# Performance work log

Hardware: AMD Instinct MI355X
Metric: run time of the kernel (lower is better)

The kernel has to match this reference:

```python
import jax, jax.numpy as jnp
import numpy as np

B, N, D, H = 4, 1024, 512, 8
DH = D // H  # per-head dim for V and for each of the two Q/K halves
LAM = 0.5


def setup_inputs() -> dict:
    key = jax.random.key(0)
    ks = jax.random.split(key, 7)
    s = 0.02
    return {
        "x": jax.random.normal(ks[0], (B, N, D), dtype=jnp.float32),
        "Wq": jax.random.normal(ks[1], (D, 2 * D), dtype=jnp.float32) * s,
        "bq": jax.random.normal(ks[2], (2 * D,), dtype=jnp.float32) * s,
        "Wk": jax.random.normal(ks[3], (D, 2 * D), dtype=jnp.float32) * s,
        "bk": jax.random.normal(ks[4], (2 * D,), dtype=jnp.float32) * s,
        "Wv": jax.random.normal(ks[5], (D, D), dtype=jnp.float32) * s,
        "bv": jax.random.normal(ks[6], (D,), dtype=jnp.float32) * s,
    }


def reference(x, Wq, bq, Wk, bk, Wv, bv):
    b, n, d = x.shape
    q = (x @ Wq + bq).reshape(b, n, H, 2 * DH).transpose(0, 2, 1, 3)  # [B,H,N,2*DH]
    k = (x @ Wk + bk).reshape(b, n, H, 2 * DH).transpose(0, 2, 1, 3)
    v = (x @ Wv + bv).reshape(b, n, H, DH).transpose(0, 2, 1, 3)      # [B,H,N,DH]
    q1, q2 = q[..., :DH], q[..., DH:]
    k1, k2 = k[..., :DH], k[..., DH:]
    scale = 1.0 / jnp.sqrt(jnp.float32(DH))
    a1 = jax.nn.softmax(jnp.einsum("bhqd,bhkd->bhqk", q1, k1) * scale, axis=-1)
    a2 = jax.nn.softmax(jnp.einsum("bhqd,bhkd->bhqk", q2, k2) * scale, axis=-1)
    attn = a1 - LAM * a2                                              # [B,H,N,N]
    out = jnp.einsum("bhqk,bhkd->bhqd", attn, v)                      # [B,H,N,DH]
    return out.transpose(0, 2, 1, 3).reshape(b, n, d)
```

## Files before the change

### kernel.cpp

```cpp
#include <hip/hip_runtime.h>
#include <hip/hip_bf16.h>

typedef unsigned short u16;
typedef short s16x8 __attribute__((ext_vector_type(8)));
typedef float f32x4 __attribute__((ext_vector_type(4)));

__device__ inline u16 f2bf(float f) {
  union { float f; unsigned int u; } v; v.f = f;
  unsigned int r = v.u + 0x7fffu + ((v.u >> 16) & 1u);
  return (u16)(r >> 16);
}

__device__ __forceinline__ void g2lds16(const u16* g, u16* l) {
  __builtin_amdgcn_global_load_lds((const __attribute__((address_space(1))) void*)g,
                                   (__attribute__((address_space(3))) void*)l, 16, 0, 0);
}

__global__ __launch_bounds__(256) void prep_kernel(const float* __restrict__ x,
                                                   const float* __restrict__ Wq,
                                                   const float* __restrict__ Wk,
                                                   const float* __restrict__ Wv,
                                                   u16* __restrict__ xb, u16* __restrict__ wt) {
  __shared__ float tile[64][65];
  int bid = blockIdx.x;
  if (bid < 1024) {
    int i = (bid * 256 + threadIdx.x) * 8;
    float4 a = *(const float4*)(x + i);
    float4 b = *(const float4*)(x + i + 4);
    s16x8 o;
    o[0] = (short)f2bf(a.x); o[1] = (short)f2bf(a.y);
    o[2] = (short)f2bf(a.z); o[3] = (short)f2bf(a.w);
    o[4] = (short)f2bf(b.x); o[5] = (short)f2bf(b.y);
    o[6] = (short)f2bf(b.z); o[7] = (short)f2bf(b.w);
    *(s16x8*)(xb + i) = o;
    return;
  }
  int t = bid - 1024;
  const float* src; int C, rowoff, j0, k0;
  if (t < 256) {
    src = (t < 128) ? Wq : Wk;
    C = 1024; rowoff = (t < 128) ? 0 : 1024;
    int tt = t & 127;
    j0 = (tt & 15) * 64; k0 = (tt >> 4) * 64;
  } else {
    src = Wv; C = 512; rowoff = 2048;
    int tt = t - 256;
    j0 = (tt & 7) * 64; k0 = (tt >> 3) * 64;
  }
  int tx = threadIdx.x % 64, ty4 = threadIdx.x / 64;
#pragma unroll
  for (int p = 0; p < 16; ++p) {
    int r = p * 4 + ty4;
    tile[r][tx] = src[(size_t)(k0 + r) * C + j0 + tx];
  }
  __syncthreads();
#pragma unroll
  for (int p = 0; p < 16; ++p) {
    int r = p * 4 + ty4;
    wt[(size_t)(rowoff + j0 + r) * 512 + k0 + tx] = f2bf(tile[tx][r]);
  }
}

__global__ __launch_bounds__(256, 3) void gemm_qkv(const u16* __restrict__ xb, const u16* __restrict__ wt,
                                                   const float* __restrict__ bq, const float* __restrict__ bk,
                                                   const float* __restrict__ bv,
                                                   u16* __restrict__ qa, u16* __restrict__ ka,
                                                   u16* __restrict__ va) {
  __shared__ __align__(16) u16 As[128 * 64];
  __shared__ __align__(16) u16 Bs[128 * 64];
  int m0 = blockIdx.x * 128, j0 = blockIdx.y * 128;
  int tid = threadIdx.x;
  int w = tid >> 6, lane = tid & 63, quad = lane >> 4, l16 = lane & 15;
  int wr = (w >> 1) * 64, wc = (w & 1) * 64;

  int srow[4], scol[4], sbase[4];
#pragma unroll
  for (int it = 0; it < 4; ++it) {
    int s = it * 256 + tid;
    srow[it] = s >> 3;
    scol[it] = (s & 7) ^ ((s >> 3) & 7);
    sbase[it] = (s & ~63) * 8;
  }

  f32x4 acc[4][4];
#pragma unroll
  for (int i = 0; i < 4; ++i)
#pragma unroll
    for (int j = 0; j < 4; ++j)
#pragma unroll
      for (int r = 0; r < 4; ++r) acc[i][j][r] = 0.f;

  for (int kk = 0; kk < 8; ++kk) {
    int k0 = kk * 64;
    __syncthreads();
#pragma unroll
    for (int it = 0; it < 4; ++it) {
      g2lds16(xb + (size_t)(m0 + srow[it]) * 512 + k0 + scol[it] * 8, &As[sbase[it]]);
      g2lds16(wt + (size_t)(j0 + srow[it]) * 512 + k0 + scol[it] * 8, &Bs[sbase[it]]);
    }
    __syncthreads();
#pragma unroll
    for (int kb = 0; kb < 2; ++kb) {
      s16x8 af[4], bfr[4];
#pragma unroll
      for (int rb = 0; rb < 4; ++rb) {
        int row = wr + rb * 16 + l16;
        af[rb] = *(const s16x8*)(&As[row * 64 + (((kb * 4 + quad) ^ (row & 7)) * 8)]);
      }
#pragma unroll
      for (int cb = 0; cb < 4; ++cb) {
        int row = wc + cb * 16 + l16;
        bfr[cb] = *(const s16x8*)(&Bs[row * 64 + (((kb * 4 + quad) ^ (row & 7)) * 8)]);
      }
#pragma unroll
      for (int rb = 0; rb < 4; ++rb)
#pragma unroll
        for (int cb = 0; cb < 4; ++cb)
          acc[rb][cb] = __builtin_amdgcn_mfma_f32_16x16x32_bf16(af[rb], bfr[cb], acc[rb][cb], 0, 0, 0);
    }
  }

#pragma unroll
  for (int cb = 0; cb < 4; ++cb) {
    int j = j0 + wc + cb * 16 + l16;
    float bias = (j < 1024) ? bq[j] : (j < 2048) ? bk[j - 1024] : bv[j - 2048];
#pragma unroll
    for (int rb = 0; rb < 4; ++rb) {
#pragma unroll
      for (int r = 0; r < 4; ++r) {
        int m = m0 + wr + rb * 16 + quad * 4 + r;
        int bidx = m >> 10, n = m & 1023;
        u16 o = f2bf(acc[rb][cb][r] + bias);
        if (j < 1024) {
          int h = j >> 7, r2 = j & 127;
          qa[((size_t)((bidx * 8 + h) * 1024 + n)) * 128 + r2] = o;
        } else if (j < 2048) {
          int jj = j - 1024, h = jj >> 7, r2 = jj & 127;
          ka[((size_t)((bidx * 8 + h) * 1024 + n)) * 128 + r2] = o;
        } else {
          int jj = j - 2048, h = jj >> 6, d = jj & 63;
          va[((size_t)((bidx * 8 + h) * 64 + d)) * 1024 + n] = o;
        }
      }
    }
  }
}

__global__ __launch_bounds__(256, 2) void attn_kernel(const u16* __restrict__ qa, const u16* __restrict__ ka,
                                                      const u16* __restrict__ va, float* __restrict__ out) {
  __shared__ __align__(16) u16 smem[17408];
  u16* Ks = smem;
  u16* Vs = smem + 8192;
  u16* Ps = smem + 12288;
  float* Ex = (float*)smem;

  int bh = blockIdx.x, b = bh >> 3, h = bh & 7;
  int q0 = blockIdx.y * 32;
  int tid = threadIdx.x, w = tid >> 6, lane = tid & 63, quad = lane >> 4, l16 = lane & 15;
  int kh = w >> 1;
  int qr = q0 + (w & 1) * 16;

  const u16* kgbase = ka + (size_t)bh * 1024 * 128;
  const u16* vgbase = va + (size_t)bh * 64 * 1024;

  const u16* qrow = qa + (size_t)(bh * 1024 + qr + l16) * 128;
  s16x8 qf[2][2];
  qf[0][0] = *(const s16x8*)(qrow + quad * 8);
  qf[0][1] = *(const s16x8*)(qrow + 32 + quad * 8);
  qf[1][0] = *(const s16x8*)(qrow + 64 + quad * 8);
  qf[1][1] = *(const s16x8*)(qrow + 96 + quad * 8);

  f32x4 O1[5], O2[5];
#pragma unroll
  for (int i = 0; i < 5; ++i)
#pragma unroll
    for (int r = 0; r < 4; ++r) { O1[i][r] = 0.f; O2[i][r] = 0.f; }

  s16x8 onesf;
#pragma unroll
  for (int i = 0; i < 8; ++i) onesf[i] = (l16 == 0) ? (short)0x3F80 : (short)0;

  size_t kgo[4]; int kbse[4];
#pragma unroll
  for (int i = 0; i < 4; ++i) {
    int s = i * 256 + tid;
    int skh = s >> 9, row = (s >> 4) & 31, c = s & 15;
    kgo[i] = (size_t)(skh * 512 + row) * 128 + ((c ^ (row & 7)) * 8);
    kbse[i] = (s & ~63) * 8;
  }
  size_t vgo[2]; int vbse[2];
#pragma unroll
  for (int i = 0; i < 2; ++i) {
    int s = i * 256 + tid;
    int skh = s >> 8, row = (s >> 2) & 63, c = s & 3;
    vgo[i] = (size_t)row * 1024 + skh * 512 + ((c ^ (row & 3)) * 8);
    vbse[i] = (s & ~63) * 8;
  }

  for (int kt = 0; kt < 16; ++kt) {
    __syncthreads();
#pragma unroll
    for (int i = 0; i < 4; ++i)
      g2lds16(kgbase + kgo[i] + (size_t)kt * 4096, &Ks[kbse[i]]);
#pragma unroll
    for (int i = 0; i < 2; ++i)
      g2lds16(vgbase + vgo[i] + (size_t)kt * 32, &Vs[vbse[i]]);
    __syncthreads();

    s16x8 vf[4];
#pragma unroll
    for (int ct = 0; ct < 4; ++ct) {
      int row = ct * 16 + l16;
      vf[ct] = *(const s16x8*)(&Vs[kh * 2048 + row * 32 + ((quad ^ (row & 3)) * 8)]);
    }

#pragma unroll
    for (int hh = 0; hh < 2; ++hh) {
#pragma unroll
      for (int nt = 0; nt < 2; ++nt) {
        f32x4 sv; sv[0] = sv[1] = sv[2] = sv[3] = 0.f;
#pragma unroll
        for (int kb = 0; kb < 2; ++kb) {
          int row = nt * 16 + l16;
          s16x8 kf = *(const s16x8*)(&Ks[kh * 4096 + row * 128 +
                                         (((hh * 8 + kb * 4 + quad) ^ (row & 7)) * 8)]);
          sv = __builtin_amdgcn_mfma_f32_16x16x32_bf16(qf[hh][kb], kf, sv, 0, 0, 0);
        }
#pragma unroll
        for (int r = 0; r < 4; ++r)
          Ps[((w * 2 + hh) * 16 + quad * 4 + r) * 40 + nt * 16 + l16] = f2bf(__expf(sv[r] * 0.125f));
      }
    }
    asm volatile("s_waitcnt lgkmcnt(0)" ::: "memory");
    s16x8 pf0 = *(const s16x8*)(&Ps[((w * 2 + 0) * 16 + l16) * 40 + quad * 8]);
    s16x8 pf1 = *(const s16x8*)(&Ps[((w * 2 + 1) * 16 + l16) * 40 + quad * 8]);
#pragma unroll
    for (int ct = 0; ct < 5; ++ct) {
      s16x8 bfr = (ct < 4) ? vf[ct] : onesf;
      O1[ct] = __builtin_amdgcn_mfma_f32_16x16x32_bf16(pf0, bfr, O1[ct], 0, 0, 0);
      O2[ct] = __builtin_amdgcn_mfma_f32_16x16x32_bf16(pf1, bfr, O2[ct], 0, 0, 0);
    }
  }
  __syncthreads();

  if (w >= 2) {
    int wi = w - 2;
#pragma unroll
    for (int ct = 0; ct < 4; ++ct)
#pragma unroll
      for (int r = 0; r < 4; ++r) {
        Ex[((wi * 2 + 0) * 16 + quad * 4 + r) * 68 + ct * 16 + l16] = O1[ct][r];
        Ex[((wi * 2 + 1) * 16 + quad * 4 + r) * 68 + ct * 16 + l16] = O2[ct][r];
      }
    if (l16 == 0) {
#pragma unroll
      for (int r = 0; r < 4; ++r) {
        Ex[((wi * 2 + 0) * 16 + quad * 4 + r) * 68 + 64] = O1[4][r];
        Ex[((wi * 2 + 1) * 16 + quad * 4 + r) * 68 + 64] = O2[4][r];
      }
    }
  }
  __syncthreads();
  if (w < 2) {
#pragma unroll
    for (int ct = 0; ct < 4; ++ct)
#pragma unroll
      for (int r = 0; r < 4; ++r) {
        O1[ct][r] += Ex[((w * 2 + 0) * 16 + quad * 4 + r) * 68 + ct * 16 + l16];
        O2[ct][r] += Ex[((w * 2 + 1) * 16 + quad * 4 + r) * 68 + ct * 16 + l16];
      }
    if (l16 == 0) {
#pragma unroll
      for (int r = 0; r < 4; ++r) {
        O1[4][r] += Ex[((w * 2 + 0) * 16 + quad * 4 + r) * 68 + 64];
        O2[4][r] += Ex[((w * 2 + 1) * 16 + quad * 4 + r) * 68 + 64];
      }
    }
    float inv1[4], inv2[4];
#pragma unroll
    for (int r = 0; r < 4; ++r) {
      float l1 = __shfl(O1[4][r], lane & 48, 64);
      float l2 = __shfl(O2[4][r], lane & 48, 64);
      inv1[r] = 1.0f / l1;
      inv2[r] = 1.0f / l2;
    }
    int nb = qr + quad * 4;
#pragma unroll
    for (int ct = 0; ct < 4; ++ct)
#pragma unroll
      for (int r = 0; r < 4; ++r) {
        float val = O1[ct][r] * inv1[r] - 0.5f * O2[ct][r] * inv2[r];
        out[(size_t)(b * 1024 + nb + r) * 512 + h * 64 + ct * 16 + l16] = val;
      }
  }
}

extern "C" void kernel_launch(void* const* d_in, const int* in_sizes, int n_in,
                              void* d_out, int out_size, void* d_ws, size_t ws_size,
                              hipStream_t stream) {
  (void)in_sizes; (void)n_in; (void)out_size; (void)ws_size;
  const float* x  = (const float*)d_in[0];
  const float* Wq = (const float*)d_in[1];
  const float* bq = (const float*)d_in[2];
  const float* Wk = (const float*)d_in[3];
  const float* bk = (const float*)d_in[4];
  const float* Wv = (const float*)d_in[5];
  const float* bv = (const float*)d_in[6];
  float* out = (float*)d_out;

  char* ws = (char*)d_ws;
  u16* xb = (u16*)(ws);
  u16* wt = (u16*)(ws + 4194304);
  u16* qa = (u16*)(ws + 6815744);
  u16* ka = (u16*)(ws + 15204352);
  u16* va = (u16*)(ws + 23592960);

  prep_kernel<<<1344, 256, 0, stream>>>(x, Wq, Wk, Wv, xb, wt);
  gemm_qkv<<<dim3(32, 20), 256, 0, stream>>>(xb, wt, bq, bk, bv, qa, ka, va);
  attn_kernel<<<dim3(32, 32), 256, 0, stream>>>(qa, ka, va, out);
}
```

Before: 140.0 us.

## Keep attention probabilities in registers via transposed MFMA and lane shuffles

The QK^T MFMA operands are swapped so each lane holds scores for one query row. The exp values are truncated to bf16, packed, and redistributed with cross-lane shuffles into the B-operand layout for the PV MFMA, which removes the LDS round trip for P and the extra ones-column MFMA used for the row sums. Row sums are now accumulated in registers and combined with xor shuffles, and the output is written as float4 stores. This cuts LDS traffic, a waitcnt stall, and shared memory size, at the cost of several shuffles per tile and bf16 truncation instead of rounding for P.

```diff
diff --git a/kernel.cpp b/kernel.cpp
--- a/kernel.cpp
+++ b/kernel.cpp
@@ -2,6 +2,7 @@
 #include <hip/hip_bf16.h>
 
 typedef unsigned short u16;
+typedef unsigned int u32;
 typedef short s16x8 __attribute__((ext_vector_type(8)));
 typedef float f32x4 __attribute__((ext_vector_type(4)));
 
@@ -148,10 +149,9 @@
 
 __global__ __launch_bounds__(256, 2) void attn_kernel(const u16* __restrict__ qa, const u16* __restrict__ ka,
                                                       const u16* __restrict__ va, float* __restrict__ out) {
-  __shared__ __align__(16) u16 smem[17408];
+  __shared__ __align__(16) u16 smem[12288];
   u16* Ks = smem;
   u16* Vs = smem + 8192;
-  u16* Ps = smem + 12288;
   float* Ex = (float*)smem;
 
   int bh = blockIdx.x, b = bh >> 3, h = bh & 7;
@@ -170,15 +170,12 @@
   qf[1][0] = *(const s16x8*)(qrow + 64 + quad * 8);
   qf[1][1] = *(const s16x8*)(qrow + 96 + quad * 8);
 
-  f32x4 O1[5], O2[5];
-#pragma unroll
-  for (int i = 0; i < 5; ++i)
+  f32x4 O1[4], O2[4];
+#pragma unroll
+  for (int i = 0; i < 4; ++i)
 #pragma unroll
     for (int r = 0; r < 4; ++r) { O1[i][r] = 0.f; O2[i][r] = 0.f; }
-
-  s16x8 onesf;
-#pragma unroll
-  for (int i = 0; i < 8; ++i) onesf[i] = (l16 == 0) ? (short)0x3F80 : (short)0;
+  float lacc[2] = {0.f, 0.f};
 
   size_t kgo[4]; int kbse[4];
 #pragma unroll
@@ -197,6 +194,10 @@
     vbse[i] = (s & ~63) * 8;
   }
 
+  int srcLo = (quad & 1) * 32 + l16;
+  int srcHi = srcLo + 16;
+  bool hiSel = quad >= 2;
+
   for (int kt = 0; kt < 16; ++kt) {
     __syncthreads();
 #pragma unroll
@@ -216,6 +217,7 @@
 
 #pragma unroll
     for (int hh = 0; hh < 2; ++hh) {
+      u32 pk[2][2];
 #pragma unroll
       for (int nt = 0; nt < 2; ++nt) {
         f32x4 sv; sv[0] = sv[1] = sv[2] = sv[3] = 0.f;
@@ -224,74 +226,77 @@
           int row = nt * 16 + l16;
           s16x8 kf = *(const s16x8*)(&Ks[kh * 4096 + row * 128 +
                                          (((hh * 8 + kb * 4 + quad) ^ (row & 7)) * 8)]);
-          sv = __builtin_amdgcn_mfma_f32_16x16x32_bf16(qf[hh][kb], kf, sv, 0, 0, 0);
+          sv = __builtin_amdgcn_mfma_f32_16x16x32_bf16(kf, qf[hh][kb], sv, 0, 0, 0);
         }
-#pragma unroll
-        for (int r = 0; r < 4; ++r)
-          Ps[((w * 2 + hh) * 16 + quad * 4 + r) * 40 + nt * 16 + l16] = f2bf(__expf(sv[r] * 0.125f));
-      }
-    }
-    asm volatile("s_waitcnt lgkmcnt(0)" ::: "memory");
-    s16x8 pf0 = *(const s16x8*)(&Ps[((w * 2 + 0) * 16 + l16) * 40 + quad * 8]);
-    s16x8 pf1 = *(const s16x8*)(&Ps[((w * 2 + 1) * 16 + l16) * 40 + quad * 8]);
-#pragma unroll
-    for (int ct = 0; ct < 5; ++ct) {
-      s16x8 bfr = (ct < 4) ? vf[ct] : onesf;
-      O1[ct] = __builtin_amdgcn_mfma_f32_16x16x32_bf16(pf0, bfr, O1[ct], 0, 0, 0);
-      O2[ct] = __builtin_amdgcn_mfma_f32_16x16x32_bf16(pf1, bfr, O2[ct], 0, 0, 0);
+        u32 ue[4];
+#pragma unroll
+        for (int r = 0; r < 4; ++r) {
+          float e = __expf(sv[r] * 0.125f);
+          ue[r] = __float_as_uint(e);
+          lacc[hh] += __uint_as_float(ue[r] & 0xffff0000u);
+        }
+        pk[nt][0] = (ue[0] >> 16) | (ue[1] & 0xffff0000u);
+        pk[nt][1] = (ue[2] >> 16) | (ue[3] & 0xffff0000u);
+      }
+      u32 a0 = __shfl(pk[0][0], srcLo), b0 = __shfl(pk[1][0], srcLo);
+      u32 a1 = __shfl(pk[0][1], srcLo), b1 = __shfl(pk[1][1], srcLo);
+      u32 a2 = __shfl(pk[0][0], srcHi), b2 = __shfl(pk[1][0], srcHi);
+      u32 a3 = __shfl(pk[0][1], srcHi), b3 = __shfl(pk[1][1], srcHi);
+      union { u32 wv[4]; s16x8 frag; } pu;
+      pu.wv[0] = hiSel ? b0 : a0;
+      pu.wv[1] = hiSel ? b1 : a1;
+      pu.wv[2] = hiSel ? b2 : a2;
+      pu.wv[3] = hiSel ? b3 : a3;
+      if (hh == 0) {
+#pragma unroll
+        for (int ct = 0; ct < 4; ++ct)
+          O1[ct] = __builtin_amdgcn_mfma_f32_16x16x32_bf16(vf[ct], pu.frag, O1[ct], 0, 0, 0);
+      } else {
+#pragma unroll
+        for (int ct = 0; ct < 4; ++ct)
+          O2[ct] = __builtin_amdgcn_mfma_f32_16x16x32_bf16(vf[ct], pu.frag, O2[ct], 0, 0, 0);
+      }
     }
   }
   __syncthreads();
 
   if (w >= 2) {
-    int wi = w - 2;
+    int base = ((w - 2) * 64 + lane) * 35;
 #pragma unroll
     for (int ct = 0; ct < 4; ++ct)
 #pragma unroll
       for (int r = 0; r < 4; ++r) {
-        Ex[((wi * 2 + 0) * 16 + quad * 4 + r) * 68 + ct * 16 + l16] = O1[ct][r];
-        Ex[((wi * 2 + 1) * 16 + quad * 4 + r) * 68 + ct * 16 + l16] = O2[ct][r];
-      }
-    if (l16 == 0) {
-#pragma unroll
-      for (int r = 0; r < 4; ++r) {
-        Ex[((wi * 2 + 0) * 16 + quad * 4 + r) * 68 + 64] = O1[4][r];
-        Ex[((wi * 2 + 1) * 16 + quad * 4 + r) * 68 + 64] = O2[4][r];
-      }
-    }
+        Ex[base + ct * 4 + r] = O1[ct][r];
+        Ex[base + 16 + ct * 4 + r] = O2[ct][r];
+      }
+    Ex[base + 32] = lacc[0];
+    Ex[base + 33] = lacc[1];
   }
   __syncthreads();
   if (w < 2) {
+    int base = (w * 64 + lane) * 35;
 #pragma unroll
     for (int ct = 0; ct < 4; ++ct)
 #pragma unroll
       for (int r = 0; r < 4; ++r) {
-        O1[ct][r] += Ex[((w * 2 + 0) * 16 + quad * 4 + r) * 68 + ct * 16 + l16];
-        O2[ct][r] += Ex[((w * 2 + 1) * 16 + quad * 4 + r) * 68 + ct * 16 + l16];
-      }
-    if (l16 == 0) {
-#pragma unroll
-      for (int r = 0; r < 4; ++r) {
-        O1[4][r] += Ex[((w * 2 + 0) * 16 + quad * 4 + r) * 68 + 64];
-        O2[4][r] += Ex[((w * 2 + 1) * 16 + quad * 4 + r) * 68 + 64];
-      }
-    }
-    float inv1[4], inv2[4];
-#pragma unroll
-    for (int r = 0; r < 4; ++r) {
-      float l1 = __shfl(O1[4][r], lane & 48, 64);
-      float l2 = __shfl(O2[4][r], lane & 48, 64);
-      inv1[r] = 1.0f / l1;
-      inv2[r] = 1.0f / l2;
-    }
-    int nb = qr + quad * 4;
-#pragma unroll
-    for (int ct = 0; ct < 4; ++ct)
-#pragma unroll
-      for (int r = 0; r < 4; ++r) {
-        float val = O1[ct][r] * inv1[r] - 0.5f * O2[ct][r] * inv2[r];
-        out[(size_t)(b * 1024 + nb + r) * 512 + h * 64 + ct * 16 + l16] = val;
-      }
+        O1[ct][r] += Ex[base + ct * 4 + r];
+        O2[ct][r] += Ex[base + 16 + ct * 4 + r];
+      }
+    float l1 = lacc[0] + Ex[base + 32];
+    float l2 = lacc[1] + Ex[base + 33];
+    l1 += __shfl_xor(l1, 16); l1 += __shfl_xor(l1, 32);
+    l2 += __shfl_xor(l2, 16); l2 += __shfl_xor(l2, 32);
+    float inv1 = 1.0f / l1, inv2 = 1.0f / l2;
+    float* orow = out + (size_t)(b * 1024 + qr + l16) * 512 + h * 64;
+#pragma unroll
+    for (int ct = 0; ct < 4; ++ct) {
+      float4 v;
+      v.x = O1[ct][0] * inv1 - 0.5f * O2[ct][0] * inv2;
+      v.y = O1[ct][1] * inv1 - 0.5f * O2[ct][1] * inv2;
+      v.z = O1[ct][2] * inv1 - 0.5f * O2[ct][2] * inv2;
+      v.w = O1[ct][3] * inv1 - 0.5f * O2[ct][3] * inv2;
+      *(float4*)(orow + ct * 16 + quad * 4) = v;
+    }
   }
 }
 
```

Result: no change. 139.4 us (-0.4%).
